# Optimization experiments

Measured on AMD Instinct MI355X. Metric: run time of the kernel, lower is better.

The kernel has to match this reference:

```python
import jax, jax.numpy as jnp
import numpy as np

N_HEADS, BUCKET, N_HASHES, DIM = 8, 25, 4, 128
PKM_TOPK = 16
NEG = -1e9
SELF_VAL = -5e4

def layer_norm(x, g, b, eps=1e-5):
    m = jnp.mean(x, -1, keepdims=True)
    v = jnp.mean(jnp.square(x - m), -1, keepdims=True)
    return (x - m) * jax.lax.rsqrt(v + eps) * g + b

def pos_encoding(S, d):
    pos = jnp.arange(S, dtype=jnp.float32)[:, None]
    div = jnp.exp(jnp.arange(0, d, 2, dtype=jnp.float32) * (-9.21034037198 / d))
    pe = jnp.zeros((S, d), jnp.float32)
    pe = pe.at[:, 0::2].set(jnp.sin(pos * div))
    pe = pe.at[:, 1::2].set(jnp.cos(pos * div))
    return pe

def look_back(t):
    # concat each chunk with the previous chunk along the within-chunk axis
    return jnp.concatenate([t, jnp.roll(t, 1, axis=1)], axis=2)

def lsh_attend(qk, v, keep, rot):
    # qk, v: [BH, S, D]; keep: [BH, S] bool; rot: [D, R, n_buckets//2]
    BH, S, D = qk.shape
    R = rot.shape[1]
    nb = 2 * rot.shape[2]
    kn = qk * jax.lax.rsqrt(jnp.sum(jnp.square(qk), -1, keepdims=True) + 1e-9)  # shared-QK keys are unit length
    rotated = jnp.einsum('bsd,drn->brsn', qk, rot)
    buckets = jnp.argmax(jnp.concatenate([rotated, -rotated], -1), axis=-1)  # [BH, R, S]
    buckets = buckets + (jnp.arange(R) * nb)[None, :, None]  # offset per hash round
    buckets = buckets.reshape(BH, R * S)
    pos = jnp.arange(R * S) % S
    perm = jnp.argsort(buckets * S + pos[None, :], axis=-1)  # stable sort by (bucket, position)
    undo = jnp.argsort(perm, axis=-1)
    st = perm % S  # original token position of each sorted slot
    gather = lambda t: jnp.take_along_axis(t, st[:, :, None], axis=1)
    c = BUCKET
    nc = (R * S) // c
    sq = gather(qk).reshape(BH, nc, c, D)
    sk = gather(kn).reshape(BH, nc, c, D)
    sv = gather(v).reshape(BH, nc, c, D)
    sm = jnp.take_along_axis(keep, st, axis=1).reshape(BH, nc, c)
    t_q = st.reshape(BH, nc, c)
    bk, bv = look_back(sk), look_back(sv)
    t_kv, m_kv = look_back(t_q), look_back(sm)
    dots = jnp.einsum('bncd,bnkd->bnck', sq, bk) * (D ** -0.5)  # [BH, nc, c, 2c]
    pair = sm[..., :, None] & m_kv[..., None, :]
    dots = jnp.where(pair, dots, NEG)                                   # padding mask
    dots = jnp.where(t_q[..., :, None] < t_kv[..., None, :], NEG, dots)  # causal
    dots = jnp.where(t_q[..., :, None] == t_kv[..., None, :], SELF_VAL, dots)  # discourage self-attn
    lse = jax.nn.logsumexp(dots, axis=-1, keepdims=True)
    attn = jnp.exp(dots - lse)
    bo = jnp.einsum('bnck,bnkd->bncd', attn, bv)
    so = bo.reshape(BH, R * S, D)
    slse = lse.reshape(BH, R * S)
    o = jnp.take_along_axis(so, undo[:, :, None], axis=1).reshape(BH, R, S, D)
    lu = jnp.take_along_axis(slse, undo, axis=1).reshape(BH, R, S)
    w = jax.nn.softmax(lu, axis=1)[..., None]  # combine hash rounds by their logsumexp
    return jnp.sum(o * w, axis=1)

def lsh_self_attention(x, keep, Wqk, Wv, Wo, bo, rot):
    B, S, dim = x.shape
    H = N_HEADS
    Dh = dim // H
    split = lambda t: t.reshape(B, S, H, Dh).transpose(0, 2, 1, 3).reshape(B * H, S, Dh)
    qk, v = split(x @ Wqk), split(x @ Wv)
    keep_bh = jnp.repeat(keep, H, axis=0)
    o = lsh_attend(qk, v, keep_bh, rot)
    o = o.reshape(B, H, S, Dh).transpose(0, 2, 1, 3).reshape(B, S, dim)
    return o @ Wo + bo

def pkm(x, Wq, keys, values):
    # keys: [H, nk, 2, dh]; values: [nk*nk, dim] (product-key memory)
    B, S, dim = x.shape
    H, nk, _, dh = keys.shape
    q = (x @ Wq).reshape(B, S, H, 2, dh)
    dots = jnp.einsum('bshpd,hnpd->bshpn', q, keys)
    sx, ix = jax.lax.top_k(dots[..., 0, :], PKM_TOPK)
    sy, iy = jax.lax.top_k(dots[..., 1, :], PKM_TOPK)
    alls = (sx[..., :, None] + sy[..., None, :]).reshape(B, S, H, PKM_TOPK * PKM_TOPK)
    alli = (ix[..., :, None] * nk + iy[..., None, :]).reshape(B, S, H, PKM_TOPK * PKM_TOPK)
    fs, p = jax.lax.top_k(alls, PKM_TOPK)
    fi = jnp.take_along_axis(alli, p, axis=-1)
    attn = jax.nn.softmax(fs, -1)
    return jnp.einsum('bshk,bshkd->bsd', attn, values[fi])

def model_forward(fl, xi):
    (emb_mcc, emb_amt, emb_hour, emb_wday, rot, ln1_g, ln1_b, ln2_g, ln2_b,
     Wqk, Wv, Wo, bo, ff_w1, ff_b1, ff_w2, ff_b2, pkm_wq, pkm_keys, pkm_values,
     norm_g, norm_b, hw1, hb1, hw2_mcc, hb2_mcc, hw2_amt, hb2_amt,
     hw2_hour, hb2_hour, hw2_wday, hb2_wday) = fl
    x_mcc, x_amt, x_hour, x_wday = xi
    B, S = x_mcc.shape
    emb = jnp.concatenate([emb_mcc[x_mcc], emb_amt[x_amt], emb_hour[x_hour], emb_wday[x_wday]], axis=-1)
    emb = emb + pos_encoding(S, DIM)[None]
    keep = x_mcc != 0
    # reversible reformer: x1 = x1 + attn(ln(x2)); x2 = x2 + ff_or_pkm(ln(x1)); out = mean of halves
    x1 = x2 = emb
    ffi = pki = 0
    for l in range(8):
        h = layer_norm(x2, ln1_g[l], ln1_b[l])
        x1 = x1 + lsh_self_attention(h, keep, Wqk[l], Wv[l], Wo[l], bo[l], rot)
        h2 = layer_norm(x1, ln2_g[l], ln2_b[l])
        if l in (3, 6):  # pkm_layers = (4, 7), 1-indexed
            x2 = x2 + pkm(h2, pkm_wq[pki], pkm_keys[pki], pkm_values[pki])
            pki += 1
        else:
            x2 = x2 + (jax.nn.gelu(h2 @ ff_w1[ffi] + ff_b1[ffi], approximate=False) @ ff_w2[ffi] + ff_b2[ffi])
            ffi += 1
    y = layer_norm((x1 + x2) * 0.5, norm_g, norm_b)
    outs = []
    for i, (w2, b2) in enumerate([(hw2_mcc, hb2_mcc), (hw2_amt, hb2_amt), (hw2_hour, hb2_hour), (hw2_wday, hb2_wday)]):
        h = jax.nn.gelu(y @ hw1[i] + hb1[i], approximate=False)
        outs.append(h @ w2 + b2)
    return tuple(outs)

def setup_inputs() -> dict:
    key = jax.random.key(0)
    ks = iter(jax.random.split(key, 64))
    B, S = 16, 1000
    nrm = lambda *s: jax.random.normal(next(ks), s, jnp.float32) * 0.02
    inp = dict(
        x_mcc=jax.random.randint(next(ks), (B, S), 0, 350),
        x_amt=jax.random.randint(next(ks), (B, S), 0, 100),
        x_hour=jax.random.randint(next(ks), (B, S), 0, 25),
        x_wday=jax.random.randint(next(ks), (B, S), 0, 8),
        emb_mcc=nrm(350, 64), emb_amt=nrm(100, 32), emb_hour=nrm(25, 16), emb_wday=nrm(8, 16),
        rot=jax.random.normal(next(ks), (16, N_HASHES, 20), jnp.float32),  # [dim_head, rounds, n_buckets//2]
        ln1_g=jnp.ones((8, 128)), ln1_b=jnp.zeros((8, 128)),
        ln2_g=jnp.ones((8, 128)), ln2_b=jnp.zeros((8, 128)),
        Wqk=nrm(8, 128, 128), Wv=nrm(8, 128, 128), Wo=nrm(8, 128, 128), bo=jnp.zeros((8, 128)),
        ff_w1=nrm(6, 128, 512), ff_b1=jnp.zeros((6, 512)), ff_w2=nrm(6, 512, 128), ff_b2=jnp.zeros((6, 128)),
        pkm_wq=nrm(2, 128, 512), pkm_keys=nrm(2, 4, 128, 2, 64), pkm_values=nrm(2, 16384, 128),
        norm_g=jnp.ones((128,)), norm_b=jnp.zeros((128,)),
        hw1=nrm(4, 128, 128), hb1=jnp.zeros((4, 128)),
        hw2_mcc=nrm(128, 350), hb2_mcc=jnp.zeros((350,)),
        hw2_amt=nrm(128, 100), hb2_amt=jnp.zeros((100,)),
        hw2_hour=nrm(128, 25), hb2_hour=jnp.zeros((25,)),
        hw2_wday=nrm(128, 8), hb2_wday=jnp.zeros((8,)),
    )
    return inp

def reference(x_mcc, x_amt, x_hour, x_wday, emb_mcc, emb_amt, emb_hour, emb_wday, rot,
              ln1_g, ln1_b, ln2_g, ln2_b, Wqk, Wv, Wo, bo,
              ff_w1, ff_b1, ff_w2, ff_b2, pkm_wq, pkm_keys, pkm_values,
              norm_g, norm_b, hw1, hb1, hw2_mcc, hb2_mcc, hw2_amt, hb2_amt,
              hw2_hour, hb2_hour, hw2_wday, hb2_wday):
    fl = (emb_mcc, emb_amt, emb_hour, emb_wday, rot, ln1_g, ln1_b, ln2_g, ln2_b,
          Wqk, Wv, Wo, bo, ff_w1, ff_b1, ff_w2, ff_b2, pkm_wq, pkm_keys, pkm_values,
          norm_g, norm_b, hw1, hb1, hw2_mcc, hb2_mcc, hw2_amt, hb2_amt,
          hw2_hour, hb2_hour, hw2_wday, hb2_wday)
    return model_forward(fl, (x_mcc, x_amt, x_hour, x_wday))
```

## Files before the change

kernel.cpp:

```cpp
#include <hip/hip_runtime.h>
#include <math.h>

#define MM_GELU 1
#define MM_RES 2
#define MM_SPLIT 4
#define MM_SPLITONLY 8

typedef __attribute__((ext_vector_type(8))) short bfrag;
typedef __attribute__((ext_vector_type(4))) float f32x4;

__device__ inline unsigned short f2bf_rne(float f) {
  unsigned u = __float_as_uint(f);
  unsigned r = u + 0x7FFFu + ((u >> 16) & 1u);
  return (unsigned short)(r >> 16);
}
__device__ inline float bf2f(unsigned short h) {
  return __uint_as_float(((unsigned)h) << 16);
}

__global__ __launch_bounds__(128) void embed_kernel(
    const int* __restrict__ xm, const int* __restrict__ xa,
    const int* __restrict__ xh, const int* __restrict__ xw,
    const float* __restrict__ em, const float* __restrict__ ea,
    const float* __restrict__ eh, const float* __restrict__ ew,
    float* __restrict__ x1, float* __restrict__ x2) {
  int row = blockIdx.x;
  int d = threadIdx.x;
  int s = row % 1000;
  float v;
  if (d < 64)       v = em[xm[row]*64 + d];
  else if (d < 96)  v = ea[xa[row]*32 + (d-64)];
  else if (d < 112) v = eh[xh[row]*16 + (d-96)];
  else              v = ew[xw[row]*16 + (d-112)];
  int i = d >> 1;
  float dv = expf((float)(2*i) * (-9.21034037198f/128.f));
  float ang = (float)s * dv;
  v += (d & 1) ? cosf(ang) : sinf(ang);
  x1[row*128 + d] = v;
  x2[row*128 + d] = v;
}

__global__ __launch_bounds__(256) void ln_kernel(
    const float* __restrict__ x, const float* __restrict__ xb,
    const float* __restrict__ g, const float* __restrict__ b,
    unsigned short* __restrict__ oh, unsigned short* __restrict__ ol) {
  int row = blockIdx.x * 4 + (threadIdx.x >> 6);
  int t = threadIdx.x & 63;
  float v0 = x[row*128 + t], v1 = x[row*128 + 64 + t];
  if (xb) { v0 = 0.5f*(v0 + xb[row*128 + t]); v1 = 0.5f*(v1 + xb[row*128 + 64 + t]); }
  float sum = v0 + v1;
  #pragma unroll
  for (int o = 32; o > 0; o >>= 1) sum += __shfl_xor(sum, o);
  float mean = sum * (1.f/128.f);
  float d0 = v0 - mean, d1 = v1 - mean;
  float vs = d0*d0 + d1*d1;
  #pragma unroll
  for (int o = 32; o > 0; o >>= 1) vs += __shfl_xor(vs, o);
  float rstd = rsqrtf(vs*(1.f/128.f) + 1e-5f);
  float y0 = d0*rstd*g[t]    + b[t];
  float y1 = d1*rstd*g[t+64] + b[t+64];
  unsigned short h0 = f2bf_rne(y0), h1 = f2bf_rne(y1);
  oh[row*128 + t]      = h0;
  ol[row*128 + t]      = f2bf_rne(y0 - bf2f(h0));
  oh[row*128 + 64 + t] = h1;
  ol[row*128 + 64 + t] = f2bf_rne(y1 - bf2f(h1));
}

__global__ __launch_bounds__(256) void splitT_kernel(
    const float* __restrict__ src, unsigned short* __restrict__ hiT,
    unsigned short* __restrict__ loT, int K, int N,
    long srcStride, long dstStride) {
  src += (size_t)blockIdx.z * srcStride;
  hiT += (size_t)blockIdx.z * dstStride;
  loT += (size_t)blockIdx.z * dstStride;
  int n0 = blockIdx.x * 64, k0 = blockIdx.y * 64;
  __shared__ unsigned short sH[64][68], sL[64][68];
  int tid = threadIdx.x;
  int c = tid & 63, r4 = tid >> 6;
  #pragma unroll
  for (int rr = 0; rr < 16; ++rr) {
    int r = r4 + rr*4;
    float val = (n0 + c < N) ? src[(size_t)(k0 + r)*N + n0 + c] : 0.f;
    unsigned short h = f2bf_rne(val);
    sH[r][c] = h;
    sL[r][c] = f2bf_rne(val - bf2f(h));
  }
  __syncthreads();
  #pragma unroll
  for (int rr = 0; rr < 16; ++rr) {
    int n = r4 + rr*4;
    if (n0 + n < N) {
      hiT[(size_t)(n0 + n)*K + k0 + c] = sH[c][n];
      loT[(size_t)(n0 + n)*K + k0 + c] = sL[c][n];
    }
  }
}

__global__ __launch_bounds__(256) void mm_bf16_kernel(
    const unsigned short* __restrict__ Ah, const unsigned short* __restrict__ Al,
    const unsigned short* __restrict__ BhT, const unsigned short* __restrict__ BlT,
    const float* __restrict__ bias, float* __restrict__ C,
    unsigned short* __restrict__ Ch, unsigned short* __restrict__ Cl,
    int M, int N, int K, int flags) {
  __shared__ __align__(16) unsigned short sAh[64][72], sAl[64][72], sBh[64][72], sBl[64][72];
  int tid = threadIdx.x;
  int bm = blockIdx.x * 64, bn = blockIdx.y * 64;
  int w = tid >> 6, lane = tid & 63;
  int l15 = lane & 15, kg = lane >> 4;
  f32x4 acc[4];
  #pragma unroll
  for (int t = 0; t < 4; ++t) { acc[t][0]=0.f; acc[t][1]=0.f; acc[t][2]=0.f; acc[t][3]=0.f; }

  for (int k0 = 0; k0 < K; k0 += 64) {
    #pragma unroll
    for (int uu = 0; uu < 2; ++uu) {
      int u = tid + uu*256;
      int rr = u >> 3, cc = u & 7;
      size_t ga = (size_t)(bm + rr)*K + k0 + cc*8;
      *(bfrag*)&sAh[rr][cc*8] = *(const bfrag*)(Ah + ga);
      *(bfrag*)&sAl[rr][cc*8] = *(const bfrag*)(Al + ga);
      int n = bn + rr;
      if (n < N) {
        size_t gb = (size_t)n*K + k0 + cc*8;
        *(bfrag*)&sBh[rr][cc*8] = *(const bfrag*)(BhT + gb);
        *(bfrag*)&sBl[rr][cc*8] = *(const bfrag*)(BlT + gb);
      } else {
        bfrag z = {0,0,0,0,0,0,0,0};
        *(bfrag*)&sBh[rr][cc*8] = z;
        *(bfrag*)&sBl[rr][cc*8] = z;
      }
    }
    __syncthreads();
    #pragma unroll
    for (int ks = 0; ks < 2; ++ks) {
      int am = w*16 + l15;
      bfrag a_h = *(const bfrag*)&sAh[am][ks*32 + kg*8];
      bfrag a_l = *(const bfrag*)&sAl[am][ks*32 + kg*8];
      #pragma unroll
      for (int t = 0; t < 4; ++t) {
        int nn = t*16 + l15;
        bfrag b_h = *(const bfrag*)&sBh[nn][ks*32 + kg*8];
        bfrag b_l = *(const bfrag*)&sBl[nn][ks*32 + kg*8];
        acc[t] = __builtin_amdgcn_mfma_f32_16x16x32_bf16(a_h, b_h, acc[t], 0, 0, 0);
        acc[t] = __builtin_amdgcn_mfma_f32_16x16x32_bf16(a_h, b_l, acc[t], 0, 0, 0);
        acc[t] = __builtin_amdgcn_mfma_f32_16x16x32_bf16(a_l, b_h, acc[t], 0, 0, 0);
      }
    }
    __syncthreads();
  }
  #pragma unroll
  for (int t = 0; t < 4; ++t) {
    int col = bn + t*16 + l15;
    if (col < N) {
      #pragma unroll
      for (int r = 0; r < 4; ++r) {
        int row = bm + w*16 + kg*4 + r;
        float val = acc[t][r];
        if (bias) val += bias[col];
        if (flags & MM_GELU) val = 0.5f*val*(1.f + erff(val*0.70710678118f));
        size_t oi;
        if (flags & MM_SPLIT) {
          int bb = row / 1000, ss = row % 1000;
          int hd = col >> 4, dd = col & 15;
          oi = (((size_t)(bb*8 + hd))*1000 + ss)*16 + dd;
        } else {
          oi = (size_t)row*N + col;
        }
        if (flags & MM_SPLITONLY) {
          unsigned short h = f2bf_rne(val);
          Ch[oi] = h;
          Cl[oi] = f2bf_rne(val - bf2f(h));
        } else if (flags & MM_RES) C[oi] += val;
        else C[oi] = val;
      }
    }
  }
}

__global__ __launch_bounds__(256) void bucket_kernel(
    const float* __restrict__ qk, const float* __restrict__ rot,
    int* __restrict__ buckets) {
  int idx = blockIdx.x*256 + threadIdx.x;
  if (idx >= 128000) return;
  int bh = idx / 1000, s = idx % 1000;
  float q[16];
  #pragma unroll
  for (int d = 0; d < 16; ++d) q[d] = qk[(bh*1000+s)*16 + d];
  #pragma unroll 1
  for (int r = 0; r < 4; ++r) {
    float rv[20];
    #pragma unroll
    for (int n = 0; n < 20; ++n) {
      float acc = 0.f;
      #pragma unroll
      for (int d = 0; d < 16; ++d) acc += q[d]*rot[(d*4 + r)*20 + n];
      rv[n] = acc;
    }
    float best = -INFINITY; int bi = 0;
    #pragma unroll
    for (int n = 0; n < 40; ++n) {
      float val = (n < 20) ? rv[n] : -rv[n-20];
      if (val > best) { best = val; bi = n; }
    }
    buckets[(bh*4 + r)*1000 + s] = bi;
  }
}

__global__ __launch_bounds__(64) void sort_kernel(
    const int* __restrict__ buckets, int* __restrict__ st, int* __restrict__ undo) {
  int bh = blockIdx.x >> 2;
  int r = blockIdx.x & 3;
  const int* bkt = buckets + (bh*4 + r)*1000;
  __shared__ int off[40];
  int lane = threadIdx.x;
  if (lane < 40) off[lane] = 0;
  __syncthreads();
  unsigned long long below = (lane == 63) ? 0x7FFFFFFFFFFFFFFFull : ((1ull << lane) - 1ull);
  for (int c = 0; c < 16; ++c) {
    int s = c*64 + lane;
    bool valid = (s < 1000);
    int b = valid ? bkt[s] : 0;
    unsigned long long mask = __ballot(valid);
    #pragma unroll
    for (int bit = 0; bit < 6; ++bit) {
      unsigned long long vote = __ballot((b >> bit) & 1);
      mask &= ((b >> bit) & 1) ? vote : ~vote;
    }
    if (valid) {
      int rank = (int)__popcll(mask & below);
      if (rank == 0) off[b] += (int)__popcll(mask);
    }
    __syncthreads();
  }
  if (lane == 0) {
    int acc = 0;
    for (int bb = 0; bb < 40; ++bb) { int cn = off[bb]; off[bb] = acc; acc += cn; }
  }
  __syncthreads();
  int base = bh*4000 + r*1000;
  for (int c = 0; c < 16; ++c) {
    int s = c*64 + lane;
    bool valid = (s < 1000);
    int b = valid ? bkt[s] : 0;
    unsigned long long mask = __ballot(valid);
    #pragma unroll
    for (int bit = 0; bit < 6; ++bit) {
      unsigned long long vote = __ballot((b >> bit) & 1);
      mask &= ((b >> bit) & 1) ? vote : ~vote;
    }
    if (valid) {
      int myoff = off[b];
      int rank = (int)__popcll(mask & below);
      int slot = myoff + rank;
      st[base + slot] = s;
      undo[base + s] = r*1000 + slot;
      if (rank == 0) off[b] = myoff + (int)__popcll(mask);
    }
    __syncthreads();
  }
}

__global__ __launch_bounds__(64) void attn_chunk_kernel(
    const float* __restrict__ qk, const float* __restrict__ v,
    const int* __restrict__ st, const int* __restrict__ xm,
    float* __restrict__ so, float* __restrict__ slse) {
  int blk = blockIdx.x;
  int bh = blk / 160;
  int n = blk % 160;
  int b = bh >> 3;
  int lane = threadIdx.x;
  __shared__ __align__(16) float RAW[50][20];
  __shared__ __align__(16) float BV[50][20];
  __shared__ float RSQ[50];
  __shared__ int TKV[50], MKV[50];
  int pn = (n + 159) % 160;
  if (lane < 50) {
    int slot = (lane < 25) ? (n*25 + lane) : (pn*25 + (lane - 25));
    int t = st[bh*4000 + slot];
    TKV[lane] = t;
    MKV[lane] = (xm[b*1000 + t] != 0) ? 1 : 0;
  }
  __syncthreads();
  for (int e = lane; e < 200; e += 64) {
    int rr = e >> 2, j = (e & 3) * 4;
    int t = TKV[rr];
    const float* qr = qk + ((size_t)bh*1000 + t)*16 + j;
    const float* vr = v  + ((size_t)bh*1000 + t)*16 + j;
    *(float4*)&RAW[rr][j] = *(const float4*)qr;
    *(float4*)&BV[rr][j]  = *(const float4*)vr;
  }
  __syncthreads();
  if (lane < 50) {
    float ss = 1e-9f;
    #pragma unroll
    for (int d = 0; d < 16; ++d) ss += RAW[lane][d]*RAW[lane][d];
    RSQ[lane] = rsqrtf(ss);
  }
  __syncthreads();
  if (lane < 50) {
    int q = lane % 25, h = lane / 25;
    int partner = (h == 0) ? lane + 25 : lane - 25;
    float sq[16];
    #pragma unroll
    for (int j = 0; j < 4; ++j) {
      float4 f = *(const float4*)&RAW[q][j*4];
      sq[j*4+0]=f.x; sq[j*4+1]=f.y; sq[j*4+2]=f.z; sq[j*4+3]=f.w;
    }
    int tq = TKV[q], mq = MKV[q];
    float p[25];
    #pragma unroll
    for (int i = 0; i < 25; ++i) {
      int k = h*25 + i;
      float acc = 0.f;
      #pragma unroll
      for (int j = 0; j < 4; ++j) {
        float4 f = *(const float4*)&RAW[k][j*4];
        acc += sq[j*4+0]*f.x + sq[j*4+1]*f.y + sq[j*4+2]*f.z + sq[j*4+3]*f.w;
      }
      acc *= 0.25f * RSQ[k];
      int tk = TKV[k], mk = MKV[k];
      if (!(mq && mk)) acc = -1e9f;
      if (tq < tk) acc = -1e9f;
      if (tq == tk) acc = -5e4f;
      p[i] = acc;
    }
    float m = -INFINITY;
    #pragma unroll
    for (int i = 0; i < 25; ++i) m = fmaxf(m, p[i]);
    m = fmaxf(m, __shfl(m, partner));
    float S = 0.f;
    #pragma unroll
    for (int i = 0; i < 25; ++i) { p[i] = expf(p[i] - m); S += p[i]; }
    S += __shfl(S, partner);
    float lse = m + logf(S);
    float rS = 1.f / S;
    float o[16];
    #pragma unroll
    for (int d = 0; d < 16; ++d) o[d] = 0.f;
    #pragma unroll
    for (int i = 0; i < 25; ++i) {
      int k = h*25 + i;
      float wt = p[i];
      #pragma unroll
      for (int j = 0; j < 4; ++j) {
        float4 f = *(const float4*)&BV[k][j*4];
        o[j*4+0] += wt*f.x; o[j*4+1] += wt*f.y; o[j*4+2] += wt*f.z; o[j*4+3] += wt*f.w;
      }
    }
    #pragma unroll
    for (int d = 0; d < 16; ++d) o[d] += __shfl(o[d], partner);
    if (h == 0) {
      int slot = n*25 + q;
      float* op = so + ((size_t)bh*4000 + slot)*16;
      #pragma unroll
      for (int j = 0; j < 4; ++j) {
        float4 f;
        f.x = o[j*4+0]*rS; f.y = o[j*4+1]*rS; f.z = o[j*4+2]*rS; f.w = o[j*4+3]*rS;
        *(float4*)(op + j*4) = f;
      }
      slse[bh*4000 + slot] = lse;
    }
  }
}

__global__ __launch_bounds__(256) void combine_kernel(
    const float* __restrict__ so, const float* __restrict__ slse,
    const int* __restrict__ undo, unsigned short* __restrict__ aoh,
    unsigned short* __restrict__ aol) {
  int idx = blockIdx.x*256 + threadIdx.x;
  if (idx >= 2048000) return;
  int d = idx & 15;
  int s = (idx >> 4) % 1000;
  int bh = idx / 16000;
  int b = bh >> 3, hd = bh & 7;
  int s0 = undo[bh*4000 + s];
  int s1 = undo[bh*4000 + 1000 + s];
  int s2 = undo[bh*4000 + 2000 + s];
  int s3 = undo[bh*4000 + 3000 + s];
  float l0 = slse[bh*4000 + s0], l1 = slse[bh*4000 + s1];
  float l2 = slse[bh*4000 + s2], l3 = slse[bh*4000 + s3];
  float m = fmaxf(fmaxf(l0,l1), fmaxf(l2,l3));
  float w0 = expf(l0-m), w1 = expf(l1-m), w2 = expf(l2-m), w3 = expf(l3-m);
  float rs = 1.f/(w0+w1+w2+w3);
  const float* base = so + (size_t)bh*4000*16;
  float o = (w0*base[s0*16+d] + w1*base[s1*16+d] + w2*base[s2*16+d] + w3*base[s3*16+d]) * rs;
  size_t oi = ((size_t)b*1000 + s)*128 + hd*16 + d;
  unsigned short h = f2bf_rne(o);
  aoh[oi] = h;
  aol[oi] = f2bf_rne(o - bf2f(h));
}

__global__ __launch_bounds__(256) void pkm_m_kernel(
    const float* __restrict__ Wq, const float* __restrict__ keys,
    float* __restrict__ M) {
  int hp = blockIdx.x;
  int h = hp >> 1, p = hp & 1;
  int tid = threadIdx.x;
  __shared__ float Ks[128][65];
  for (int e = tid; e < 8192; e += 256) {
    int n = e >> 6, d = e & 63;
    Ks[n][d] = keys[((size_t)(h*128 + n)*2 + p)*64 + d];
  }
  __syncthreads();
  int k = tid >> 1;
  int nbase = (tid & 1) * 64;
  float wk[64];
  const float* wq = Wq + (size_t)k*512 + h*128 + p*64;
  #pragma unroll
  for (int d = 0; d < 64; ++d) wk[d] = wq[d];
  for (int n = 0; n < 64; ++n) {
    int nn = nbase + n;
    float acc = 0.f;
    #pragma unroll
    for (int d = 0; d < 64; ++d) acc += wk[d]*Ks[nn][d];
    M[(size_t)k*1024 + hp*128 + nn] = acc;
  }
}

__device__ inline unsigned long long pk_key(float v, int idx) {
  unsigned u = __float_as_uint(v);
  u = (u & 0x80000000u) ? ~u : (u | 0x80000000u);
  unsigned kv = ~u;
  return ((unsigned long long)kv << 32) | (unsigned)idx;
}
__device__ inline float pk_val(unsigned long long key) {
  unsigned m = ~(unsigned)(key >> 32);
  return (m & 0x80000000u) ? __uint_as_float(m & 0x7FFFFFFFu) : __uint_as_float(~m);
}

__global__ __launch_bounds__(256) void pkm_select_kernel(
    const float* __restrict__ dots, const float* __restrict__ values,
    float* __restrict__ x2out) {
  int row = blockIdx.x;
  int tid = threadIdx.x;
  int h = tid >> 6;
  int lane = tid & 63;
  __shared__ float OUT[4][128];
  const float* dr = dots + (size_t)row*1024 + h*256;
  unsigned long long x0 = pk_key(dr[lane], lane);
  unsigned long long x1 = pk_key(dr[64 + lane], 64 + lane);
  unsigned long long y0 = pk_key(dr[128 + lane], lane);
  unsigned long long y1 = pk_key(dr[192 + lane], 64 + lane);
  #pragma unroll 1
  for (int k = 2; k <= 128; k <<= 1) {
    #pragma unroll 1
    for (int j = k >> 1; j >= 1; j >>= 1) {
      if (j == 64) {
        unsigned long long lo, hi;
        lo = (x0 < x1) ? x0 : x1; hi = (x0 < x1) ? x1 : x0; x0 = lo; x1 = hi;
        lo = (y0 < y1) ? y0 : y1; hi = (y0 < y1) ? y1 : y0; y0 = lo; y1 = hi;
      } else {
        unsigned long long px0 = __shfl_xor(x0, j);
        unsigned long long px1 = __shfl_xor(x1, j);
        unsigned long long py0 = __shfl_xor(y0, j);
        unsigned long long py1 = __shfl_xor(y1, j);
        bool low = ((lane & j) == 0);
        bool up0 = ((lane & k) == 0);
        bool up1 = (((lane + 64) & k) == 0);
        bool d0 = (low == up0);
        bool d1 = (low == up1);
        if (d0 ? (px0 < x0) : (px0 > x0)) x0 = px0;
        if (d1 ? (px1 < x1) : (px1 > x1)) x1 = px1;
        if (d0 ? (py0 < y0) : (py0 > y0)) y0 = py0;
        if (d1 ? (py1 < y1) : (py1 > y1)) y1 = py1;
      }
    }
  }
  float xv = pk_val(x0);
  float yv = pk_val(y0);
  int xi = (int)(unsigned)(x0 & 0xFFFFFFFFull);
  int yi = (int)(unsigned)(y0 & 0xFFFFFFFFull);
  int kx, ky;
  if      (lane < 16) { kx = 0; ky = lane; }
  else if (lane < 24) { kx = 1; ky = lane - 16; }
  else if (lane < 29) { kx = 2; ky = lane - 24; }
  else if (lane < 33) { kx = 3; ky = lane - 29; }
  else if (lane < 36) { kx = 4; ky = lane - 33; }
  else if (lane < 38) { kx = 5; ky = lane - 36; }
  else if (lane < 40) { kx = 6; ky = lane - 38; }
  else if (lane < 42) { kx = 7; ky = lane - 40; }
  else                { kx = 8 + (lane - 42); ky = 0; }
  float sxk = __shfl(xv, kx);
  float syk = __shfl(yv, ky);
  unsigned long long key = (lane < 50) ? pk_key(sxk + syk, kx*16 + ky) : ~0ull;
  #pragma unroll 1
  for (int k = 2; k <= 64; k <<= 1) {
    #pragma unroll 1
    for (int j = k >> 1; j >= 1; j >>= 1) {
      unsigned long long pk = __shfl_xor(key, j);
      bool low = ((lane & j) == 0);
      bool up = ((lane & k) == 0);
      bool take = (low == up) ? (pk < key) : (pk > key);
      if (take) key = pk;
    }
  }
  float myv = pk_val(key);
  int pos = (int)(key & 0xFFull);
  int ix = __shfl(xi, pos >> 4);
  int iy = __shfl(yi, pos & 15);
  int myfi = ix*128 + iy;
  float fs0 = __shfl(myv, 0);
  float osum0 = 0.f, osum1 = 0.f, wsum = 0.f;
  #pragma unroll
  for (int k = 0; k < 16; ++k) {
    float fv = __shfl(myv, k);
    int fik = __shfl(myfi, k);
    float wgk = expf(fv - fs0);
    wsum += wgk;
    const float* vr = values + (size_t)fik * 128;
    osum0 += wgk * vr[lane];
    osum1 += wgk * vr[lane + 64];
  }
  float rs = 1.f / wsum;
  OUT[h][lane] = osum0 * rs;
  OUT[h][lane + 64] = osum1 * rs;
  __syncthreads();
  if (tid < 128) {
    float r = OUT[0][tid] + OUT[1][tid] + OUT[2][tid] + OUT[3][tid];
    x2out[(size_t)row*128 + tid] += r;
  }
}

extern "C" void kernel_launch(void* const* d_in, const int* in_sizes, int n_in,
                              void* d_out, int out_size, void* d_ws, size_t ws_size,
                              hipStream_t stream) {
  (void)in_sizes; (void)n_in; (void)out_size; (void)ws_size;
  const int* x_mcc  = (const int*)d_in[0];
  const int* x_amt  = (const int*)d_in[1];
  const int* x_hour = (const int*)d_in[2];
  const int* x_wday = (const int*)d_in[3];
  const float* emb_mcc  = (const float*)d_in[4];
  const float* emb_amt  = (const float*)d_in[5];
  const float* emb_hour = (const float*)d_in[6];
  const float* emb_wday = (const float*)d_in[7];
  const float* rot   = (const float*)d_in[8];
  const float* ln1_g = (const float*)d_in[9];
  const float* ln1_b = (const float*)d_in[10];
  const float* ln2_g = (const float*)d_in[11];
  const float* ln2_b = (const float*)d_in[12];
  const float* Wqk = (const float*)d_in[13];
  const float* Wv  = (const float*)d_in[14];
  const float* Wo  = (const float*)d_in[15];
  const float* bo  = (const float*)d_in[16];
  const float* ff_w1 = (const float*)d_in[17];
  const float* ff_b1 = (const float*)d_in[18];
  const float* ff_w2 = (const float*)d_in[19];
  const float* ff_b2 = (const float*)d_in[20];
  const float* pkm_wq   = (const float*)d_in[21];
  const float* pkm_keys = (const float*)d_in[22];
  const float* pkm_vals = (const float*)d_in[23];
  const float* norm_g = (const float*)d_in[24];
  const float* norm_b = (const float*)d_in[25];
  const float* hw1 = (const float*)d_in[26];
  const float* hb1 = (const float*)d_in[27];

  float* ws = (float*)d_ws;
  float* x1v  = ws;
  float* x2v  = ws + 2048000;
  float* hbuf = ws + 4096000;
  float* scrA = ws + 6144000;
  float* qk     = scrA;
  float* vv     = scrA + 2048000;
  float* so     = scrA + 4096000;
  float* slse   = scrA + 12288000;
  int*   buckets= (int*)(scrA + 12800000);
  int*   stp    = (int*)(scrA + 13312000);
  int*   undo   = (int*)(scrA + 13824000);
  float* attn_o = scrA + 14336000;
  float* dotsb  = scrA;
  float* Mbuf   = ws + 22528000;

  unsigned short* hbuf_h = (unsigned short*)hbuf;
  unsigned short* hbuf_l = hbuf_h + 2048000;
  unsigned short* ao_h = (unsigned short*)attn_o;
  unsigned short* ao_l = ao_h + 2048000;
  unsigned short* big_h = (unsigned short*)scrA;
  unsigned short* big_l = big_h + 8192000;
  unsigned short* hid_h = ao_h;
  unsigned short* hid_l = ao_l;

  unsigned short* wsp = (unsigned short*)(ws + 22700000);
  unsigned short* WqkT_h = wsp;
  unsigned short* WqkT_l = wsp + 131072;
  unsigned short* WvT_h  = wsp + 262144;
  unsigned short* WvT_l  = wsp + 393216;
  unsigned short* WoT_h  = wsp + 524288;
  unsigned short* WoT_l  = wsp + 655360;
  unsigned short* f1T_h  = wsp + 786432;
  unsigned short* f1T_l  = wsp + 1179648;
  unsigned short* f2T_h  = wsp + 1572864;
  unsigned short* f2T_l  = wsp + 1966080;
  unsigned short* MT_h   = wsp + 2359296;
  unsigned short* MT_l   = wsp + 2490368;
  unsigned short* hw1T_h = wsp + 2621440;
  unsigned short* hw1T_l = wsp + 2686976;
  unsigned short* h2T_h  = wsp + 2752512;
  unsigned short* h2T_l  = wsp + 2814336;

  { dim3 g(2,2,8); splitT_kernel<<<g,256,0,stream>>>(Wqk, WqkT_h, WqkT_l, 128,128, 16384,16384); }
  { dim3 g(2,2,8); splitT_kernel<<<g,256,0,stream>>>(Wv,  WvT_h,  WvT_l,  128,128, 16384,16384); }
  { dim3 g(2,2,8); splitT_kernel<<<g,256,0,stream>>>(Wo,  WoT_h,  WoT_l,  128,128, 16384,16384); }
  { dim3 g(8,2,6); splitT_kernel<<<g,256,0,stream>>>(ff_w1, f1T_h, f1T_l, 128,512, 65536,65536); }
  { dim3 g(2,8,6); splitT_kernel<<<g,256,0,stream>>>(ff_w2, f2T_h, f2T_l, 512,128, 65536,65536); }
  { dim3 g(2,2,4); splitT_kernel<<<g,256,0,stream>>>(hw1, hw1T_h, hw1T_l, 128,128, 16384,16384); }
  const float* w2s[4] = {(const float*)d_in[28], (const float*)d_in[30], (const float*)d_in[32], (const float*)d_in[34]};
  const float* b2s[4] = {(const float*)d_in[29], (const float*)d_in[31], (const float*)d_in[33], (const float*)d_in[35]};
  const int ns[4] = {350, 100, 25, 8};
  const long h2off[4] = {0, 44800, 57600, 60800};
  for (int i = 0; i < 4; ++i) {
    dim3 g((ns[i]+63)/64, 2, 1);
    splitT_kernel<<<g,256,0,stream>>>(w2s[i], h2T_h + h2off[i], h2T_l + h2off[i], 128, ns[i], 0, 0);
  }

  embed_kernel<<<16000, 128, 0, stream>>>(x_mcc, x_amt, x_hour, x_wday,
      emb_mcc, emb_amt, emb_hour, emb_wday, x1v, x2v);

  int ffi = 0, pki = 0;
  for (int l = 0; l < 8; ++l) {
    ln_kernel<<<4000, 256, 0, stream>>>(x2v, nullptr, ln1_g + l*128, ln1_b + l*128, hbuf_h, hbuf_l);
    { dim3 g(250, 2); mm_bf16_kernel<<<g, 256, 0, stream>>>(hbuf_h, hbuf_l, WqkT_h + l*16384, WqkT_l + l*16384, nullptr, qk, nullptr, nullptr, 16000, 128, 128, MM_SPLIT); }
    { dim3 g(250, 2); mm_bf16_kernel<<<g, 256, 0, stream>>>(hbuf_h, hbuf_l, WvT_h + l*16384, WvT_l + l*16384, nullptr, vv, nullptr, nullptr, 16000, 128, 128, MM_SPLIT); }
    bucket_kernel<<<500, 256, 0, stream>>>(qk, rot, buckets);
    sort_kernel<<<512, 64, 0, stream>>>(buckets, stp, undo);
    attn_chunk_kernel<<<20480, 64, 0, stream>>>(qk, vv, stp, x_mcc, so, slse);
    combine_kernel<<<8000, 256, 0, stream>>>(so, slse, undo, ao_h, ao_l);
    { dim3 g(250, 2); mm_bf16_kernel<<<g, 256, 0, stream>>>(ao_h, ao_l, WoT_h + l*16384, WoT_l + l*16384, bo + l*128, x1v, nullptr, nullptr, 16000, 128, 128, MM_RES); }
    ln_kernel<<<4000, 256, 0, stream>>>(x1v, nullptr, ln2_g + l*128, ln2_b + l*128, hbuf_h, hbuf_l);
    if (l == 3 || l == 6) {
      pkm_m_kernel<<<8, 256, 0, stream>>>(pkm_wq + (size_t)pki*65536, pkm_keys + (size_t)pki*65536, Mbuf);
      { dim3 g(16, 2, 1); splitT_kernel<<<g,256,0,stream>>>(Mbuf, MT_h, MT_l, 128, 1024, 0, 0); }
      { dim3 g(250, 16); mm_bf16_kernel<<<g, 256, 0, stream>>>(hbuf_h, hbuf_l, MT_h, MT_l, nullptr, dotsb, nullptr, nullptr, 16000, 1024, 128, 0); }
      pkm_select_kernel<<<16000, 256, 0, stream>>>(dotsb, pkm_vals + (size_t)pki*2097152, x2v);
      ++pki;
    } else {
      { dim3 g(250, 8); mm_bf16_kernel<<<g, 256, 0, stream>>>(hbuf_h, hbuf_l, f1T_h + ffi*65536, f1T_l + ffi*65536, ff_b1 + ffi*512, nullptr, big_h, big_l, 16000, 512, 128, MM_GELU|MM_SPLITONLY); }
      { dim3 g(250, 2); mm_bf16_kernel<<<g, 256, 0, stream>>>(big_h, big_l, f2T_h + ffi*65536, f2T_l + ffi*65536, ff_b2 + ffi*128, x2v, nullptr, nullptr, 16000, 128, 512, MM_RES); }
      ++ffi;
    }
  }
  ln_kernel<<<4000, 256, 0, stream>>>(x1v, x2v, norm_g, norm_b, hbuf_h, hbuf_l);

  float* out = (float*)d_out;
  size_t ooff = 0;
  for (int i = 0; i < 4; ++i) {
    { dim3 g(250, 2); mm_bf16_kernel<<<g, 256, 0, stream>>>(hbuf_h, hbuf_l, hw1T_h + i*16384, hw1T_l + i*16384, hb1 + i*128, nullptr, hid_h, hid_l, 16000, 128, 128, MM_GELU|MM_SPLITONLY); }
    { dim3 g(250, (unsigned)((ns[i]+63)/64)); mm_bf16_kernel<<<g, 256, 0, stream>>>(hid_h, hid_l, h2T_h + h2off[i], h2T_l + h2off[i], b2s[i], out + ooff, nullptr, nullptr, 16000, ns[i], 128, 0); }
    ooff += (size_t)16000 * ns[i];
  }
}
```

Baseline: 2.553 ms.

## Fuse layernorms into GEMMs, merge QK/V and head GEMMs, fuse bucket+sort, radix top-k

Layer norm is now computed inside the bf16 split GEMM prologue (per-row mean/rstd, then normalize and split on load), which removes the separate ln_kernel launches and the hbuf round trip. The QK and V projections become one N=256 GEMM, and the four head hidden GEMMs become one N=512 GEMM read with a leading dimension. Bucket hashing and sorting are merged into one kernel that keeps buckets in shared memory, with per-wave sorting that no longer needs barriers. PKM top-k replaces full bitonic sorts with a radix threshold select followed by a 16-element sort. The cost is that every N-tile of the fused GEMMs recomputes the LN statistics and conversion, adding redundant work.

```diff
diff --git a/kernel.cpp b/kernel.cpp
--- a/kernel.cpp
+++ b/kernel.cpp
@@ -5,6 +5,7 @@
 #define MM_RES 2
 #define MM_SPLIT 4
 #define MM_SPLITONLY 8
+#define MM_LNA 16
 
 typedef __attribute__((ext_vector_type(8))) short bfrag;
 typedef __attribute__((ext_vector_type(4))) float f32x4;
@@ -98,15 +99,34 @@
 
 __global__ __launch_bounds__(256) void mm_bf16_kernel(
     const unsigned short* __restrict__ Ah, const unsigned short* __restrict__ Al,
+    const float* __restrict__ Afp, const float* __restrict__ lnG, const float* __restrict__ lnB,
     const unsigned short* __restrict__ BhT, const unsigned short* __restrict__ BlT,
     const float* __restrict__ bias, float* __restrict__ C,
     unsigned short* __restrict__ Ch, unsigned short* __restrict__ Cl,
-    int M, int N, int K, int flags) {
+    int M, int N, int K, int lda, int flags) {
   __shared__ __align__(16) unsigned short sAh[64][72], sAl[64][72], sBh[64][72], sBl[64][72];
+  __shared__ float MEAN[64], RSTD[64];
   int tid = threadIdx.x;
   int bm = blockIdx.x * 64, bn = blockIdx.y * 64;
   int w = tid >> 6, lane = tid & 63;
   int l15 = lane & 15, kg = lane >> 4;
+  if (flags & MM_LNA) {
+    int rr = tid >> 2, cq = (tid & 3) * 32;
+    const float* ap = Afp + (size_t)(bm + rr)*lda + cq;
+    float s = 0.f, s2 = 0.f;
+    #pragma unroll
+    for (int j = 0; j < 8; ++j) {
+      float4 f = *(const float4*)(ap + j*4);
+      s += f.x + f.y + f.z + f.w;
+      s2 += f.x*f.x + f.y*f.y + f.z*f.z + f.w*f.w;
+    }
+    s += __shfl_xor(s, 1);  s += __shfl_xor(s, 2);
+    s2 += __shfl_xor(s2, 1); s2 += __shfl_xor(s2, 2);
+    float mean = s * (1.f/128.f);
+    float var = s2 * (1.f/128.f) - mean*mean;
+    if ((tid & 3) == 0) { MEAN[rr] = mean; RSTD[rr] = rsqrtf(var + 1e-5f); }
+    __syncthreads();
+  }
   f32x4 acc[4];
   #pragma unroll
   for (int t = 0; t < 4; ++t) { acc[t][0]=0.f; acc[t][1]=0.f; acc[t][2]=0.f; acc[t][3]=0.f; }
@@ -116,9 +136,28 @@
     for (int uu = 0; uu < 2; ++uu) {
       int u = tid + uu*256;
       int rr = u >> 3, cc = u & 7;
-      size_t ga = (size_t)(bm + rr)*K + k0 + cc*8;
-      *(bfrag*)&sAh[rr][cc*8] = *(const bfrag*)(Ah + ga);
-      *(bfrag*)&sAl[rr][cc*8] = *(const bfrag*)(Al + ga);
+      if (flags & MM_LNA) {
+        int k = k0 + cc*8;
+        const float* ap = Afp + (size_t)(bm + rr)*lda + k;
+        float4 fa = *(const float4*)(ap);
+        float4 fb = *(const float4*)(ap + 4);
+        float av8[8] = {fa.x, fa.y, fa.z, fa.w, fb.x, fb.y, fb.z, fb.w};
+        float mean = MEAN[rr], rstd = RSTD[rr];
+        bfrag vh, vl;
+        #pragma unroll
+        for (int j = 0; j < 8; ++j) {
+          float y = (av8[j] - mean)*rstd*lnG[k + j] + lnB[k + j];
+          unsigned short h = f2bf_rne(y);
+          vh[j] = (short)h;
+          vl[j] = (short)f2bf_rne(y - bf2f(h));
+        }
+        *(bfrag*)&sAh[rr][cc*8] = vh;
+        *(bfrag*)&sAl[rr][cc*8] = vl;
+      } else {
+        size_t ga = (size_t)(bm + rr)*lda + k0 + cc*8;
+        *(bfrag*)&sAh[rr][cc*8] = *(const bfrag*)(Ah + ga);
+        *(bfrag*)&sAl[rr][cc*8] = *(const bfrag*)(Al + ga);
+      }
       int n = bn + rr;
       if (n < N) {
         size_t gb = (size_t)n*K + k0 + cc*8;
@@ -161,8 +200,9 @@
         size_t oi;
         if (flags & MM_SPLIT) {
           int bb = row / 1000, ss = row % 1000;
-          int hd = col >> 4, dd = col & 15;
+          int hd = (col >> 4) & 7, dd = col & 15;
           oi = (((size_t)(bb*8 + hd))*1000 + ss)*16 + dd;
+          if (col >= 128) oi += 2048000;
         } else {
           oi = (size_t)row*N + col;
         }
@@ -177,17 +217,23 @@
   }
 }
 
-__global__ __launch_bounds__(256) void bucket_kernel(
+__global__ __launch_bounds__(128) void bucketsort_kernel(
     const float* __restrict__ qk, const float* __restrict__ rot,
-    int* __restrict__ buckets) {
-  int idx = blockIdx.x*256 + threadIdx.x;
-  if (idx >= 128000) return;
-  int bh = idx / 1000, s = idx % 1000;
-  float q[16];
-  #pragma unroll
-  for (int d = 0; d < 16; ++d) q[d] = qk[(bh*1000+s)*16 + d];
-  #pragma unroll 1
-  for (int r = 0; r < 4; ++r) {
+    int* __restrict__ st, int* __restrict__ undo) {
+  int bh = blockIdx.x >> 1;
+  int wv = threadIdx.x >> 6;
+  int r = (blockIdx.x & 1)*2 + wv;
+  int lane = threadIdx.x & 63;
+  __shared__ int bkt[2][1000];
+  __shared__ int off[2][48];
+  for (int s = lane; s < 1000; s += 64) {
+    const float* qr = qk + ((size_t)bh*1000 + s)*16;
+    float q[16];
+    #pragma unroll
+    for (int j = 0; j < 4; ++j) {
+      float4 f = *(const float4*)(qr + j*4);
+      q[j*4+0]=f.x; q[j*4+1]=f.y; q[j*4+2]=f.z; q[j*4+3]=f.w;
+    }
     float rv[20];
     #pragma unroll
     for (int n = 0; n < 20; ++n) {
@@ -202,24 +248,14 @@
       float val = (n < 20) ? rv[n] : -rv[n-20];
       if (val > best) { best = val; bi = n; }
     }
-    buckets[(bh*4 + r)*1000 + s] = bi;
-  }
-}
-
-__global__ __launch_bounds__(64) void sort_kernel(
-    const int* __restrict__ buckets, int* __restrict__ st, int* __restrict__ undo) {
-  int bh = blockIdx.x >> 2;
-  int r = blockIdx.x & 3;
-  const int* bkt = buckets + (bh*4 + r)*1000;
-  __shared__ int off[40];
-  int lane = threadIdx.x;
-  if (lane < 40) off[lane] = 0;
-  __syncthreads();
-  unsigned long long below = (lane == 63) ? 0x7FFFFFFFFFFFFFFFull : ((1ull << lane) - 1ull);
+    bkt[wv][s] = bi;
+  }
+  if (lane < 48) off[wv][lane] = 0;
+  unsigned long long below = ((1ull << lane) - 1ull);
   for (int c = 0; c < 16; ++c) {
     int s = c*64 + lane;
     bool valid = (s < 1000);
-    int b = valid ? bkt[s] : 0;
+    int b = valid ? bkt[wv][s] : 0;
     unsigned long long mask = __ballot(valid);
     #pragma unroll
     for (int bit = 0; bit < 6; ++bit) {
@@ -228,20 +264,18 @@
     }
     if (valid) {
       int rank = (int)__popcll(mask & below);
-      if (rank == 0) off[b] += (int)__popcll(mask);
-    }
-    __syncthreads();
+      if (rank == 0) off[wv][b] += (int)__popcll(mask);
+    }
   }
   if (lane == 0) {
     int acc = 0;
-    for (int bb = 0; bb < 40; ++bb) { int cn = off[bb]; off[bb] = acc; acc += cn; }
-  }
-  __syncthreads();
+    for (int bb = 0; bb < 40; ++bb) { int cn = off[wv][bb]; off[wv][bb] = acc; acc += cn; }
+  }
   int base = bh*4000 + r*1000;
   for (int c = 0; c < 16; ++c) {
     int s = c*64 + lane;
     bool valid = (s < 1000);
-    int b = valid ? bkt[s] : 0;
+    int b = valid ? bkt[wv][s] : 0;
     unsigned long long mask = __ballot(valid);
     #pragma unroll
     for (int bit = 0; bit < 6; ++bit) {
@@ -249,14 +283,13 @@
       mask &= ((b >> bit) & 1) ? vote : ~vote;
     }
     if (valid) {
-      int myoff = off[b];
+      int myoff = off[wv][b];
       int rank = (int)__popcll(mask & below);
       int slot = myoff + rank;
       st[base + slot] = s;
       undo[base + s] = r*1000 + slot;
-      if (rank == 0) off[b] = myoff + (int)__popcll(mask);
-    }
-    __syncthreads();
+      if (rank == 0) off[wv][b] = myoff + (int)__popcll(mask);
+    }
   }
 }
 
@@ -427,6 +460,10 @@
   unsigned m = ~(unsigned)(key >> 32);
   return (m & 0x80000000u) ? __uint_as_float(m & 0x7FFFFFFFu) : __uint_as_float(~m);
 }
+__device__ inline unsigned f32mono(float f) {
+  unsigned u = __float_as_uint(f);
+  return (u & 0x80000000u) ? ~u : (u | 0x80000000u);
+}
 
 __global__ __launch_bounds__(256) void pkm_select_kernel(
     const float* __restrict__ dots, const float* __restrict__ values,
@@ -435,41 +472,75 @@
   int tid = threadIdx.x;
   int h = tid >> 6;
   int lane = tid & 63;
+  __shared__ unsigned long long STG[4][2][16];
   __shared__ float OUT[4][128];
   const float* dr = dots + (size_t)row*1024 + h*256;
-  unsigned long long x0 = pk_key(dr[lane], lane);
-  unsigned long long x1 = pk_key(dr[64 + lane], 64 + lane);
-  unsigned long long y0 = pk_key(dr[128 + lane], lane);
-  unsigned long long y1 = pk_key(dr[192 + lane], 64 + lane);
-  #pragma unroll 1
-  for (int k = 2; k <= 128; k <<= 1) {
-    #pragma unroll 1
+  float vx0 = dr[lane], vx1 = dr[64 + lane];
+  float vy0 = dr[128 + lane], vy1 = dr[192 + lane];
+  unsigned mx0 = f32mono(vx0), mx1 = f32mono(vx1);
+  unsigned my0 = f32mono(vy0), my1 = f32mono(vy1);
+  unsigned long long below = ((1ull << lane) - 1ull);
+  unsigned tx = 0, ty = 0;
+  #pragma unroll
+  for (int bit = 31; bit >= 0; --bit) {
+    unsigned cx = tx | (1u << bit), cy = ty | (1u << bit);
+    int nx = (int)(__popcll(__ballot(mx0 >= cx)) + __popcll(__ballot(mx1 >= cx)));
+    int ny = (int)(__popcll(__ballot(my0 >= cy)) + __popcll(__ballot(my1 >= cy)));
+    if (nx >= 16) tx = cx;
+    if (ny >= 16) ty = cy;
+  }
+  {
+    unsigned long long g0 = __ballot(mx0 > tx), g1 = __ballot(mx1 > tx);
+    unsigned long long e0 = __ballot(mx0 == tx), e1 = __ballot(mx1 == tx);
+    int nGT = (int)(__popcll(g0) + __popcll(g1));
+    int need = 16 - nGT;
+    if (mx0 > tx) {
+      STG[h][0][(int)__popcll(g0 & below)] = pk_key(vx0, lane);
+    } else if (mx0 == tx) {
+      int er = (int)__popcll(e0 & below);
+      if (er < need) STG[h][0][nGT + er] = pk_key(vx0, lane);
+    }
+    if (mx1 > tx) {
+      STG[h][0][(int)(__popcll(g0) + __popcll(g1 & below))] = pk_key(vx1, 64 + lane);
+    } else if (mx1 == tx) {
+      int er = (int)(__popcll(e0) + __popcll(e1 & below));
+      if (er < need) STG[h][0][nGT + er] = pk_key(vx1, 64 + lane);
+    }
+  }
+  {
+    unsigned long long g0 = __ballot(my0 > ty), g1 = __ballot(my1 > ty);
+    unsigned long long e0 = __ballot(my0 == ty), e1 = __ballot(my1 == ty);
+    int nGT = (int)(__popcll(g0) + __popcll(g1));
+    int need = 16 - nGT;
+    if (my0 > ty) {
+      STG[h][1][(int)__popcll(g0 & below)] = pk_key(vy0, lane);
+    } else if (my0 == ty) {
+      int er = (int)__popcll(e0 & below);
+      if (er < need) STG[h][1][nGT + er] = pk_key(vy0, lane);
+    }
+    if (my1 > ty) {
+      STG[h][1][(int)(__popcll(g0) + __popcll(g1 & below))] = pk_key(vy1, 64 + lane);
+    } else if (my1 == ty) {
+      int er = (int)(__popcll(e0) + __popcll(e1 & below));
+      if (er < need) STG[h][1][nGT + er] = pk_key(vy1, 64 + lane);
+    }
+  }
+  unsigned long long skey = ~0ull;
+  if (lane < 32) skey = STG[h][lane >> 4][lane & 15];
+  int g16 = lane & 15;
+  #pragma unroll
+  for (int k = 2; k <= 16; k <<= 1) {
+    #pragma unroll
     for (int j = k >> 1; j >= 1; j >>= 1) {
-      if (j == 64) {
-        unsigned long long lo, hi;
-        lo = (x0 < x1) ? x0 : x1; hi = (x0 < x1) ? x1 : x0; x0 = lo; x1 = hi;
-        lo = (y0 < y1) ? y0 : y1; hi = (y0 < y1) ? y1 : y0; y0 = lo; y1 = hi;
-      } else {
-        unsigned long long px0 = __shfl_xor(x0, j);
-        unsigned long long px1 = __shfl_xor(x1, j);
-        unsigned long long py0 = __shfl_xor(y0, j);
-        unsigned long long py1 = __shfl_xor(y1, j);
-        bool low = ((lane & j) == 0);
-        bool up0 = ((lane & k) == 0);
-        bool up1 = (((lane + 64) & k) == 0);
-        bool d0 = (low == up0);
-        bool d1 = (low == up1);
-        if (d0 ? (px0 < x0) : (px0 > x0)) x0 = px0;
-        if (d1 ? (px1 < x1) : (px1 > x1)) x1 = px1;
-        if (d0 ? (py0 < y0) : (py0 > y0)) y0 = py0;
-        if (d1 ? (py1 < y1) : (py1 > y1)) y1 = py1;
-      }
-    }
-  }
-  float xv = pk_val(x0);
-  float yv = pk_val(y0);
-  int xi = (int)(unsigned)(x0 & 0xFFFFFFFFull);
-  int yi = (int)(unsigned)(y0 & 0xFFFFFFFFull);
+      unsigned long long pk2 = __shfl_xor(skey, j);
+      bool low = ((g16 & j) == 0);
+      bool up = ((g16 & k) == 0);
+      bool take = (low == up) ? (pk2 < skey) : (pk2 > skey);
+      if (take) skey = pk2;
+    }
+  }
+  float sval = pk_val(skey);
+  int sidx = (int)(unsigned)(skey & 0xFFFFFFFFull);
   int kx, ky;
   if      (lane < 16) { kx = 0; ky = lane; }
   else if (lane < 24) { kx = 1; ky = lane - 16; }
@@ -480,24 +551,42 @@
   else if (lane < 40) { kx = 6; ky = lane - 38; }
   else if (lane < 42) { kx = 7; ky = lane - 40; }
   else                { kx = 8 + (lane - 42); ky = 0; }
-  float sxk = __shfl(xv, kx);
-  float syk = __shfl(yv, ky);
-  unsigned long long key = (lane < 50) ? pk_key(sxk + syk, kx*16 + ky) : ~0ull;
-  #pragma unroll 1
-  for (int k = 2; k <= 64; k <<= 1) {
-    #pragma unroll 1
+  float cval = __shfl(sval, kx) + __shfl(sval, 16 + ky);
+  int cidx = kx*16 + ky;
+  unsigned mc = (lane < 50) ? f32mono(cval) : 0u;
+  unsigned tc = 0;
+  #pragma unroll
+  for (int bit = 31; bit >= 0; --bit) {
+    unsigned c = tc | (1u << bit);
+    if ((int)__popcll(__ballot(mc >= c)) >= 16) tc = c;
+  }
+  {
+    unsigned long long gt = __ballot(mc > tc), eq = __ballot(mc == tc);
+    int nGT = (int)__popcll(gt);
+    int need = 16 - nGT;
+    if (mc > tc) {
+      STG[h][0][(int)__popcll(gt & below)] = pk_key(cval, cidx);
+    } else if (lane < 50 && mc == tc) {
+      int er = (int)__popcll(eq & below);
+      if (er < need) STG[h][0][nGT + er] = pk_key(cval, cidx);
+    }
+  }
+  unsigned long long ck = (lane < 16) ? STG[h][0][lane] : ~0ull;
+  #pragma unroll
+  for (int k = 2; k <= 16; k <<= 1) {
+    #pragma unroll
     for (int j = k >> 1; j >= 1; j >>= 1) {
-      unsigned long long pk = __shfl_xor(key, j);
-      bool low = ((lane & j) == 0);
-      bool up = ((lane & k) == 0);
-      bool take = (low == up) ? (pk < key) : (pk > key);
-      if (take) key = pk;
-    }
-  }
-  float myv = pk_val(key);
-  int pos = (int)(key & 0xFFull);
-  int ix = __shfl(xi, pos >> 4);
-  int iy = __shfl(yi, pos & 15);
+      unsigned long long pk2 = __shfl_xor(ck, j);
+      bool low = ((g16 & j) == 0);
+      bool up = ((g16 & k) == 0);
+      bool take = (low == up) ? (pk2 < ck) : (pk2 > ck);
+      if (take) ck = pk2;
+    }
+  }
+  float myv = pk_val(ck);
+  int pos = (int)(ck & 0xFFull);
+  int ix = __shfl(sidx, pos >> 4);
+  int iy = __shfl(sidx, 16 + (pos & 15));
   int myfi = ix*128 + iy;
   float fs0 = __shfl(myv, 0);
   float osum0 = 0.f, osum1 = 0.f, wsum = 0.f;
@@ -563,7 +652,6 @@
   float* vv     = scrA + 2048000;
   float* so     = scrA + 4096000;
   float* slse   = scrA + 12288000;
-  int*   buckets= (int*)(scrA + 12800000);
   int*   stp    = (int*)(scrA + 13312000);
   int*   undo   = (int*)(scrA + 13824000);
   float* attn_o = scrA + 14336000;
@@ -576,14 +664,10 @@
   unsigned short* ao_l = ao_h + 2048000;
   unsigned short* big_h = (unsigned short*)scrA;
   unsigned short* big_l = big_h + 8192000;
-  unsigned short* hid_h = ao_h;
-  unsigned short* hid_l = ao_l;
 
   unsigned short* wsp = (unsigned short*)(ws + 22700000);
-  unsigned short* WqkT_h = wsp;
-  unsigned short* WqkT_l = wsp + 131072;
-  unsigned short* WvT_h  = wsp + 262144;
-  unsigned short* WvT_l  = wsp + 393216;
+  unsigned short* WqkvT_h = wsp;
+  unsigned short* WqkvT_l = wsp + 262144;
   unsigned short* WoT_h  = wsp + 524288;
   unsigned short* WoT_l  = wsp + 655360;
   unsigned short* f1T_h  = wsp + 786432;
@@ -597,8 +681,8 @@
   unsigned short* h2T_h  = wsp + 2752512;
   unsigned short* h2T_l  = wsp + 2814336;
 
-  { dim3 g(2,2,8); splitT_kernel<<<g,256,0,stream>>>(Wqk, WqkT_h, WqkT_l, 128,128, 16384,16384); }
-  { dim3 g(2,2,8); splitT_kernel<<<g,256,0,stream>>>(Wv,  WvT_h,  WvT_l,  128,128, 16384,16384); }
+  { dim3 g(2,2,8); splitT_kernel<<<g,256,0,stream>>>(Wqk, WqkvT_h, WqkvT_l, 128,128, 16384, 32768); }
+  { dim3 g(2,2,8); splitT_kernel<<<g,256,0,stream>>>(Wv,  WqkvT_h + 16384, WqkvT_l + 16384, 128,128, 16384, 32768); }
   { dim3 g(2,2,8); splitT_kernel<<<g,256,0,stream>>>(Wo,  WoT_h,  WoT_l,  128,128, 16384,16384); }
   { dim3 g(8,2,6); splitT_kernel<<<g,256,0,stream>>>(ff_w1, f1T_h, f1T_l, 128,512, 65536,65536); }
   { dim3 g(2,8,6); splitT_kernel<<<g,256,0,stream>>>(ff_w2, f2T_h, f2T_l, 512,128, 65536,65536); }
@@ -617,34 +701,38 @@
 
   int ffi = 0, pki = 0;
   for (int l = 0; l < 8; ++l) {
-    ln_kernel<<<4000, 256, 0, stream>>>(x2v, nullptr, ln1_g + l*128, ln1_b + l*128, hbuf_h, hbuf_l);
-    { dim3 g(250, 2); mm_bf16_kernel<<<g, 256, 0, stream>>>(hbuf_h, hbuf_l, WqkT_h + l*16384, WqkT_l + l*16384, nullptr, qk, nullptr, nullptr, 16000, 128, 128, MM_SPLIT); }
-    { dim3 g(250, 2); mm_bf16_kernel<<<g, 256, 0, stream>>>(hbuf_h, hbuf_l, WvT_h + l*16384, WvT_l + l*16384, nullptr, vv, nullptr, nullptr, 16000, 128, 128, MM_SPLIT); }
-    bucket_kernel<<<500, 256, 0, stream>>>(qk, rot, buckets);
-    sort_kernel<<<512, 64, 0, stream>>>(buckets, stp, undo);
+    { dim3 g(250, 4); mm_bf16_kernel<<<g, 256, 0, stream>>>(nullptr, nullptr, x2v, ln1_g + l*128, ln1_b + l*128,
+        WqkvT_h + l*32768, WqkvT_l + l*32768, nullptr, qk, nullptr, nullptr, 16000, 256, 128, 128, MM_SPLIT|MM_LNA); }
+    bucketsort_kernel<<<256, 128, 0, stream>>>(qk, rot, stp, undo);
     attn_chunk_kernel<<<20480, 64, 0, stream>>>(qk, vv, stp, x_mcc, so, slse);
     combine_kernel<<<8000, 256, 0, stream>>>(so, slse, undo, ao_h, ao_l);
-    { dim3 g(250, 2); mm_bf16_kernel<<<g, 256, 0, stream>>>(ao_h, ao_l, WoT_h + l*16384, WoT_l + l*16384, bo + l*128, x1v, nullptr, nullptr, 16000, 128, 128, MM_RES); }
-    ln_kernel<<<4000, 256, 0, stream>>>(x1v, nullptr, ln2_g + l*128, ln2_b + l*128, hbuf_h, hbuf_l);
+    { dim3 g(250, 2); mm_bf16_kernel<<<g, 256, 0, stream>>>(ao_h, ao_l, nullptr, nullptr, nullptr,
+        WoT_h + l*16384, WoT_l + l*16384, bo + l*128, x1v, nullptr, nullptr, 16000, 128, 128, 128, MM_RES); }
     if (l == 3 || l == 6) {
       pkm_m_kernel<<<8, 256, 0, stream>>>(pkm_wq + (size_t)pki*65536, pkm_keys + (size_t)pki*65536, Mbuf);
       { dim3 g(16, 2, 1); splitT_kernel<<<g,256,0,stream>>>(Mbuf, MT_h, MT_l, 128, 1024, 0, 0); }
-      { dim3 g(250, 16); mm_bf16_kernel<<<g, 256, 0, stream>>>(hbuf_h, hbuf_l, MT_h, MT_l, nullptr, dotsb, nullptr, nullptr, 16000, 1024, 128, 0); }
+      { dim3 g(250, 16); mm_bf16_kernel<<<g, 256, 0, stream>>>(nullptr, nullptr, x1v, ln2_g + l*128, ln2_b + l*128,
+          MT_h, MT_l, nullptr, dotsb, nullptr, nullptr, 16000, 1024, 128, 128, MM_LNA); }
       pkm_select_kernel<<<16000, 256, 0, stream>>>(dotsb, pkm_vals + (size_t)pki*2097152, x2v);
       ++pki;
     } else {
-      { dim3 g(250, 8); mm_bf16_kernel<<<g, 256, 0, stream>>>(hbuf_h, hbuf_l, f1T_h + ffi*65536, f1T_l + ffi*65536, ff_b1 + ffi*512, nullptr, big_h, big_l, 16000, 512, 128, MM_GELU|MM_SPLITONLY); }
-      { dim3 g(250, 2); mm_bf16_kernel<<<g, 256, 0, stream>>>(big_h, big_l, f2T_h + ffi*65536, f2T_l + ffi*65536, ff_b2 + ffi*128, x2v, nullptr, nullptr, 16000, 128, 512, MM_RES); }
+      { dim3 g(250, 8); mm_bf16_kernel<<<g, 256, 0, stream>>>(nullptr, nullptr, x1v, ln2_g + l*128, ln2_b + l*128,
+          f1T_h + ffi*65536, f1T_l + ffi*65536, ff_b1 + ffi*512, nullptr, big_h, big_l, 16000, 512, 128, 128, MM_GELU|MM_SPLITONLY|MM_LNA); }
+      { dim3 g(250, 2); mm_bf16_kernel<<<g, 256, 0, stream>>>(big_h, big_l, nullptr, nullptr, nullptr,
+          f2T_h + ffi*65536, f2T_l + ffi*65536, ff_b2 + ffi*128, x2v, nullptr, nullptr, 16000, 128, 512, 512, MM_RES); }
       ++ffi;
     }
   }
   ln_kernel<<<4000, 256, 0, stream>>>(x1v, x2v, norm_g, norm_b, hbuf_h, hbuf_l);
 
   float* out = (float*)d_out;
+  { dim3 g(250, 8); mm_bf16_kernel<<<g, 256, 0, stream>>>(hbuf_h, hbuf_l, nullptr, nullptr, nullptr,
+      hw1T_h, hw1T_l, hb1, nullptr, big_h, big_l, 16000, 512, 128, 128, MM_GELU|MM_SPLITONLY); }
   size_t ooff = 0;
   for (int i = 0; i < 4; ++i) {
-    { dim3 g(250, 2); mm_bf16_kernel<<<g, 256, 0, stream>>>(hbuf_h, hbuf_l, hw1T_h + i*16384, hw1T_l + i*16384, hb1 + i*128, nullptr, hid_h, hid_l, 16000, 128, 128, MM_GELU|MM_SPLITONLY); }
-    { dim3 g(250, (unsigned)((ns[i]+63)/64)); mm_bf16_kernel<<<g, 256, 0, stream>>>(hid_h, hid_l, h2T_h + h2off[i], h2T_l + h2off[i], b2s[i], out + ooff, nullptr, nullptr, 16000, ns[i], 128, 0); }
+    { dim3 g(250, (unsigned)((ns[i]+63)/64)); mm_bf16_kernel<<<g, 256, 0, stream>>>(big_h + i*128, big_l + i*128,
+        nullptr, nullptr, nullptr, h2T_h + h2off[i], h2T_l + h2off[i], b2s[i], out + ooff, nullptr, nullptr,
+        16000, ns[i], 128, 512, 0); }
     ooff += (size_t)16000 * ns[i];
   }
 }
```

New measurement: 3.275 ms. 28.3% more time.
